# Kernel optimization log

Measured on AMD Instinct MI355X. Metric: run time of the kernel, lower is better.

Reference implementation:

```python
import jax, jax.numpy as jnp
import numpy as np


def _pairwise_l2(set1, set2):
    # set1: [B, N, C], set2: [B, M, C] -> [B, N, M] Euclidean distances.
    # Equivalent to ||a - b||_2 computed via the expanded quadratic form,
    # avoiding the O(B*N*M*C) broadcasted-difference intermediate.
    sq1 = jnp.sum(set1 * set1, axis=-1)  # [B, N]
    sq2 = jnp.sum(set2 * set2, axis=-1)  # [B, M]
    inner = jnp.einsum('bnc,bmc->bnm', set1, set2)  # [B, N, M]
    d2 = sq1[:, :, None] + sq2[:, None, :] - 2.0 * inner
    return jnp.sqrt(jnp.maximum(d2, 0.0))


def reference(set1, set2):
    # mode == Hausdorff.average
    if set1.ndim == 2:
        set1 = set1[None]
    if set2.ndim == 2:
        set2 = set2[None]
    distances = _pairwise_l2(set1, set2)  # [B, N, M]
    term_1 = jnp.mean(jnp.min(distances, axis=2), axis=1)  # [B]
    term_2 = jnp.mean(jnp.min(distances, axis=1), axis=1)  # [B]
    res = term_1 + term_2
    if res.shape[0] == 1:
        res = jnp.squeeze(res, axis=0)
    return res


def setup_inputs() -> dict:
    key = jax.random.key(0)
    k1, k2 = jax.random.split(key)
    B, N, M, C = 8, 4096, 4096, 128
    set1 = jax.random.normal(k1, (B, N, C), dtype=jnp.float32)
    set2 = jax.random.normal(k2, (B, M, C), dtype=jnp.float32)
    return {"set1": set1, "set2": set2}
```

## Files before the change

kernel.cpp:

```cpp
#include <hip/hip_runtime.h>

#define B_ 8
#define N_ 4096
#define M_ 4096
#define C_ 128
#define BN_ (B_ * N_)
#define BM_ (B_ * M_)

typedef __attribute__((ext_vector_type(8))) short bf16x8;
typedef __attribute__((ext_vector_type(4))) float floatx4;
typedef __attribute__((ext_vector_type(8))) unsigned short ushort8;

__device__ __forceinline__ unsigned short f2bf(float x) {
    unsigned int u = __float_as_uint(x);
    u += 0x7FFFu + ((u >> 16) & 1u);
    return (unsigned short)(u >> 16);
}

__device__ __forceinline__ void gl2lds16(const void* g, void* l) {
    __builtin_amdgcn_global_load_lds(
        (const __attribute__((address_space(1))) void*)g,
        (__attribute__((address_space(3))) void*)l, 16, 0, 0);
}

__global__ __launch_bounds__(256) void prep_kernel(
    const float* __restrict__ S1, const float* __restrict__ S2,
    float* __restrict__ norms, unsigned short* __restrict__ bfA,
    unsigned short* __restrict__ bfB, float* __restrict__ out) {
    const int lane = threadIdx.x & 63;
    const int w    = threadIdx.x >> 6;
    const int gw   = blockIdx.x * 4 + w;
    const int r4   = lane >> 4;
    const int g4   = lane & 15;
    const int row  = gw * 4 + r4;

    const float* src = (row < BN_) ? S1 + (size_t)row * C_
                                   : S2 + (size_t)(row - BN_) * C_;
    float4 v0 = ((const float4*)src)[g4 * 2];
    float4 v1 = ((const float4*)src)[g4 * 2 + 1];

    float s = v0.x*v0.x + v0.y*v0.y + v0.z*v0.z + v0.w*v0.w
            + v1.x*v1.x + v1.y*v1.y + v1.z*v1.z + v1.w*v1.w;
    s += __shfl_xor(s, 1, 64);
    s += __shfl_xor(s, 2, 64);
    s += __shfl_xor(s, 4, 64);
    s += __shfl_xor(s, 8, 64);

    ushort8 o;
    o[0] = f2bf(v0.x); o[1] = f2bf(v0.y); o[2] = f2bf(v0.z); o[3] = f2bf(v0.w);
    o[4] = f2bf(v1.x); o[5] = f2bf(v1.y); o[6] = f2bf(v1.z); o[7] = f2bf(v1.w);

    unsigned short* dst = (row < BN_) ? bfA + (size_t)row * C_
                                      : bfB + (size_t)(row - BN_) * C_;
    *(ushort8*)&dst[(g4 ^ (row & 15)) * 8] = o;

    if (g4 == 0) norms[row] = -0.5f * s;
    if (blockIdx.x == 0 && threadIdx.x < B_) out[threadIdx.x] = 0.f;
}

__global__ __launch_bounds__(256, 2) void hausdorff_mfma(
    const unsigned short* __restrict__ Abf, const unsigned short* __restrict__ Bbf,
    const float* __restrict__ ahalf_g, const float* __restrict__ bhalf_g,
    float* __restrict__ rowpart, float* __restrict__ colpart) {

    __shared__ unsigned short B_lds[2][64 * 128];
    __shared__ float colmax_lds[4][1024];

    const int b     = blockIdx.z;
    const int x     = blockIdx.x;
    const int panel = blockIdx.y;
    const int row0  = x * 256;
    const int tid   = threadIdx.x;
    const int lane  = tid & 63;
    const int w     = tid >> 6;
    const int lm    = lane & 15;
    const int quad  = lane >> 4;
    const int wrow  = w * 64;

    const unsigned short* Aws = Abf + ((size_t)b * N_ + row0 + wrow) * C_;
    const unsigned short* Bws = Bbf + ((size_t)b * M_ + (size_t)panel * 1024) * C_;
    const float* bhalf = bhalf_g + (size_t)b * M_ + panel * 1024;

    bf16x8 af[4][4];
    #pragma unroll
    for (int i = 0; i < 4; ++i)
        #pragma unroll
        for (int c = 0; c < 4; ++c)
            af[i][c] = *(const bf16x8*)
                &Aws[(16 * i + lm) * 128 + (((c * 4 + quad) ^ lm) * 8)];

    float ha[16];
    #pragma unroll
    for (int i = 0; i < 4; ++i) {
        float4 t = *(const float4*)&ahalf_g[(size_t)b * N_ + row0 + wrow + 16 * i + 4 * quad];
        ha[4*i+0] = t.x; ha[4*i+1] = t.y; ha[4*i+2] = t.z; ha[4*i+3] = t.w;
    }

    float rv[16];
    #pragma unroll
    for (int v = 0; v < 16; ++v) rv[v] = -1e30f;

    #pragma unroll
    for (int k = 0; k < 4; ++k) {
        const int off = w * 2048 + k * 512;
        gl2lds16(Bws + off + lane * 8, &B_lds[0][off]);
    }

    for (int it = 0; it < 16; ++it) {
        const int cur = it & 1;
        __syncthreads();

        if (it < 15) {
            const unsigned short* Bt = Bws + (size_t)(it + 1) * 64 * C_;
            #pragma unroll
            for (int k = 0; k < 4; ++k) {
                const int off = w * 2048 + k * 512;
                gl2lds16(Bt + off + lane * 8, &B_lds[cur ^ 1][off]);
            }
        }

        float hb[4];
        #pragma unroll
        for (int j = 0; j < 4; ++j)
            hb[j] = bhalf[it * 64 + 16 * j + lm];

        floatx4 acc[4][4];
        #pragma unroll
        for (int i = 0; i < 4; ++i)
            #pragma unroll
            for (int j = 0; j < 4; ++j)
                #pragma unroll
                for (int r = 0; r < 4; ++r)
                    acc[i][j][r] = ha[4 * i + r] + hb[j];

        #pragma unroll
        for (int h = 0; h < 2; ++h) {
            bf16x8 bfr[2][4];
            #pragma unroll
            for (int j2 = 0; j2 < 2; ++j2)
                #pragma unroll
                for (int c = 0; c < 4; ++c)
                    bfr[j2][c] = *(const bf16x8*)
                        &B_lds[cur][(16 * (2 * h + j2) + lm) * 128 +
                                    (((c * 4 + quad) ^ lm) * 8)];
            #pragma unroll
            for (int c = 0; c < 4; ++c)
                #pragma unroll
                for (int i = 0; i < 4; ++i)
                    #pragma unroll
                    for (int j2 = 0; j2 < 2; ++j2)
                        acc[i][2 * h + j2] = __builtin_amdgcn_mfma_f32_16x16x32_bf16(
                            af[i][c], bfr[j2][c], acc[i][2 * h + j2], 0, 0, 0);
        }

        #pragma unroll
        for (int i = 0; i < 4; ++i)
            #pragma unroll
            for (int r = 0; r < 4; ++r) {
                float m01 = fmaxf(acc[i][0][r], acc[i][1][r]);
                float m23 = fmaxf(acc[i][2][r], acc[i][3][r]);
                rv[4 * i + r] = fmaxf(rv[4 * i + r], fmaxf(m01, m23));
            }

        #pragma unroll
        for (int j = 0; j < 4; ++j) {
            float t0 = fmaxf(fmaxf(acc[0][j][0], acc[0][j][1]),
                             fmaxf(acc[0][j][2], acc[0][j][3]));
            float t1 = fmaxf(fmaxf(acc[1][j][0], acc[1][j][1]),
                             fmaxf(acc[1][j][2], acc[1][j][3]));
            float t2 = fmaxf(fmaxf(acc[2][j][0], acc[2][j][1]),
                             fmaxf(acc[2][j][2], acc[2][j][3]));
            float t3 = fmaxf(fmaxf(acc[3][j][0], acc[3][j][1]),
                             fmaxf(acc[3][j][2], acc[3][j][3]));
            float cv = fmaxf(fmaxf(t0, t1), fmaxf(t2, t3));
            cv = fmaxf(cv, __shfl_xor(cv, 16, 64));
            cv = fmaxf(cv, __shfl_xor(cv, 32, 64));
            if (quad == 0)
                colmax_lds[w][it * 64 + 16 * j + lm] = cv;
        }
    }

    #pragma unroll
    for (int s = 1; s < 16; s <<= 1)
        #pragma unroll
        for (int v = 0; v < 16; ++v)
            rv[v] = fmaxf(rv[v], __shfl_xor(rv[v], s, 64));
    if (lm == 0) {
        #pragma unroll
        for (int v = 0; v < 16; ++v)
            rowpart[((size_t)panel * B_ + b) * N_ + row0 + wrow +
                    16 * (v >> 2) + 4 * quad + (v & 3)] = rv[v];
    }

    __syncthreads();

    {
        const int c = tid * 4;
        float4 a0 = *(const float4*)&colmax_lds[0][c];
        float4 a1 = *(const float4*)&colmax_lds[1][c];
        float4 a2 = *(const float4*)&colmax_lds[2][c];
        float4 a3 = *(const float4*)&colmax_lds[3][c];
        float4 r;
        r.x = fmaxf(fmaxf(a0.x, a1.x), fmaxf(a2.x, a3.x));
        r.y = fmaxf(fmaxf(a0.y, a1.y), fmaxf(a2.y, a3.y));
        r.z = fmaxf(fmaxf(a0.z, a1.z), fmaxf(a2.z, a3.z));
        r.w = fmaxf(fmaxf(a0.w, a1.w), fmaxf(a2.w, a3.w));
        *(float4*)&colpart[((size_t)x * B_ + b) * M_ + (size_t)panel * 1024 + c] = r;
    }
}

__global__ __launch_bounds__(256) void hausdorff_reduce(
    const float* __restrict__ rowpart, const float* __restrict__ colpart,
    float* __restrict__ out) {
    __shared__ float ws4[4];
    const int b    = blockIdx.x >> 3;
    const int part = blockIdx.x & 7;
    const int base = part * 512;
    float s = 0.f;
    for (int i = base + (int)threadIdx.x; i < base + 512; i += 256) {
        float ra = fmaxf(rowpart[((size_t)0 * B_ + b) * N_ + i],
                         rowpart[((size_t)1 * B_ + b) * N_ + i]);
        float rb = fmaxf(rowpart[((size_t)2 * B_ + b) * N_ + i],
                         rowpart[((size_t)3 * B_ + b) * N_ + i]);
        float rm = fmaxf(ra, rb);
        float ca = -1e30f, cb = -1e30f;
        #pragma unroll
        for (int xx = 0; xx < 16; xx += 2) {
            ca = fmaxf(ca, colpart[((size_t)xx * B_ + b) * M_ + i]);
            cb = fmaxf(cb, colpart[((size_t)(xx + 1) * B_ + b) * M_ + i]);
        }
        float cm = fmaxf(ca, cb);
        s += sqrtf(fmaxf(-2.f * rm, 0.f)) * (1.f / N_)
           + sqrtf(fmaxf(-2.f * cm, 0.f)) * (1.f / M_);
    }
    #pragma unroll
    for (int off = 32; off > 0; off >>= 1) s += __shfl_down(s, off, 64);
    if ((threadIdx.x & 63) == 0) ws4[threadIdx.x >> 6] = s;
    __syncthreads();
    if (threadIdx.x == 0)
        atomicAdd(&out[b], ws4[0] + ws4[1] + ws4[2] + ws4[3]);
}

extern "C" void kernel_launch(void* const* d_in, const int* in_sizes, int n_in,
                              void* d_out, int out_size, void* d_ws, size_t ws_size,
                              hipStream_t stream) {
    const float* s1 = (const float*)d_in[0];
    const float* s2 = (const float*)d_in[1];
    float* out = (float*)d_out;

    float* norms         = (float*)d_ws;
    unsigned short* bfA  = (unsigned short*)(norms + BN_ + BM_);
    unsigned short* bfB  = bfA + (size_t)BN_ * C_;
    float* rowpart       = (float*)(bfB + (size_t)BM_ * C_);
    float* colpart       = rowpart + (size_t)4 * B_ * N_;

    prep_kernel<<<(BN_ + BM_) / 16, 256, 0, stream>>>(
        s1, s2, norms, bfA, bfB, out);

    dim3 grid(N_ / 256, M_ / 1024, B_);
    hausdorff_mfma<<<grid, 256, 0, stream>>>(
        bfA, bfB, norms, norms + BN_, rowpart, colpart);

    hausdorff_reduce<<<B_ * 8, 256, 0, stream>>>(rowpart, colpart, out);
}
```

Measured before the change: 121.4 us.

## Process two B tiles per barrier with 4-slot LDS ring and MFMA priority

The main loop now handles two 64-row B tiles per iteration, using a four-buffer LDS ring so each barrier covers two tiles and prefetches the next pair. MFMA sections are wrapped in s_setprio to favour matrix issue, and the prep kernel processes four rows per wave with a quarter of the blocks. The aim is fewer barriers and more latency hiding. The cost is doubled LDS for B (64KB plus colmax), which may limit occupancy to fewer than 2 blocks per CU, and more register pressure.

```diff
diff --git a/kernel.cpp b/kernel.cpp
--- a/kernel.cpp
+++ b/kernel.cpp
@@ -29,41 +29,109 @@
     unsigned short* __restrict__ bfB, float* __restrict__ out) {
     const int lane = threadIdx.x & 63;
     const int w    = threadIdx.x >> 6;
-    const int gw   = blockIdx.x * 4 + w;
     const int r4   = lane >> 4;
     const int g4   = lane & 15;
-    const int row  = gw * 4 + r4;
-
-    const float* src = (row < BN_) ? S1 + (size_t)row * C_
-                                   : S2 + (size_t)(row - BN_) * C_;
-    float4 v0 = ((const float4*)src)[g4 * 2];
-    float4 v1 = ((const float4*)src)[g4 * 2 + 1];
-
-    float s = v0.x*v0.x + v0.y*v0.y + v0.z*v0.z + v0.w*v0.w
-            + v1.x*v1.x + v1.y*v1.y + v1.z*v1.z + v1.w*v1.w;
-    s += __shfl_xor(s, 1, 64);
-    s += __shfl_xor(s, 2, 64);
-    s += __shfl_xor(s, 4, 64);
-    s += __shfl_xor(s, 8, 64);
-
-    ushort8 o;
-    o[0] = f2bf(v0.x); o[1] = f2bf(v0.y); o[2] = f2bf(v0.z); o[3] = f2bf(v0.w);
-    o[4] = f2bf(v1.x); o[5] = f2bf(v1.y); o[6] = f2bf(v1.z); o[7] = f2bf(v1.w);
-
-    unsigned short* dst = (row < BN_) ? bfA + (size_t)row * C_
-                                      : bfB + (size_t)(row - BN_) * C_;
-    *(ushort8*)&dst[(g4 ^ (row & 15)) * 8] = o;
-
-    if (g4 == 0) norms[row] = -0.5f * s;
+
+    #pragma unroll
+    for (int step = 0; step < 4; ++step) {
+        const int row = blockIdx.x * 64 + step * 16 + w * 4 + r4;
+
+        const float* src = (row < BN_) ? S1 + (size_t)row * C_
+                                       : S2 + (size_t)(row - BN_) * C_;
+        float4 v0 = ((const float4*)src)[g4 * 2];
+        float4 v1 = ((const float4*)src)[g4 * 2 + 1];
+
+        float s = v0.x*v0.x + v0.y*v0.y + v0.z*v0.z + v0.w*v0.w
+                + v1.x*v1.x + v1.y*v1.y + v1.z*v1.z + v1.w*v1.w;
+        s += __shfl_xor(s, 1, 64);
+        s += __shfl_xor(s, 2, 64);
+        s += __shfl_xor(s, 4, 64);
+        s += __shfl_xor(s, 8, 64);
+
+        ushort8 o;
+        o[0] = f2bf(v0.x); o[1] = f2bf(v0.y);
+        o[2] = f2bf(v0.z); o[3] = f2bf(v0.w);
+        o[4] = f2bf(v1.x); o[5] = f2bf(v1.y);
+        o[6] = f2bf(v1.z); o[7] = f2bf(v1.w);
+
+        unsigned short* dst = (row < BN_) ? bfA + (size_t)row * C_
+                                          : bfB + (size_t)(row - BN_) * C_;
+        *(ushort8*)&dst[(g4 ^ (row & 15)) * 8] = o;
+
+        if (g4 == 0) norms[row] = -0.5f * s;
+    }
     if (blockIdx.x == 0 && threadIdx.x < B_) out[threadIdx.x] = 0.f;
 }
+
+
+#define COMPUTE_TILE(t_, buf_)                                                \
+  do {                                                                        \
+    const int tt_ = (t_);                                                     \
+    float hb_[4];                                                             \
+    _Pragma("unroll")                                                         \
+    for (int j_ = 0; j_ < 4; ++j_)                                            \
+        hb_[j_] = bhalf[tt_ * 64 + 16 * j_ + lm];                             \
+    floatx4 acc_[4][4];                                                       \
+    _Pragma("unroll")                                                         \
+    for (int i_ = 0; i_ < 4; ++i_)                                            \
+      _Pragma("unroll")                                                       \
+      for (int j_ = 0; j_ < 4; ++j_)                                          \
+        _Pragma("unroll")                                                     \
+        for (int r_ = 0; r_ < 4; ++r_)                                        \
+            acc_[i_][j_][r_] = ha[4 * i_ + r_] + hb_[j_];                     \
+    _Pragma("unroll")                                                         \
+    for (int h_ = 0; h_ < 2; ++h_) {                                          \
+      bf16x8 bfr_[2][4];                                                      \
+      _Pragma("unroll")                                                       \
+      for (int j2_ = 0; j2_ < 2; ++j2_)                                       \
+        _Pragma("unroll")                                                     \
+        for (int c_ = 0; c_ < 4; ++c_)                                        \
+          bfr_[j2_][c_] = *(const bf16x8*)                                    \
+              &B_lds[buf_][(16 * (2 * h_ + j2_) + lm) * 128 +                 \
+                           (((c_ * 4 + quad) ^ lm) * 8)];                     \
+      __builtin_amdgcn_s_setprio(1);                                          \
+      _Pragma("unroll")                                                       \
+      for (int c_ = 0; c_ < 4; ++c_)                                          \
+        _Pragma("unroll")                                                     \
+        for (int i_ = 0; i_ < 4; ++i_)                                        \
+          _Pragma("unroll")                                                   \
+          for (int j2_ = 0; j2_ < 2; ++j2_)                                   \
+            acc_[i_][2 * h_ + j2_] = __builtin_amdgcn_mfma_f32_16x16x32_bf16( \
+                af[i_][c_], bfr_[j2_][c_], acc_[i_][2 * h_ + j2_], 0, 0, 0);  \
+      __builtin_amdgcn_s_setprio(0);                                          \
+    }                                                                         \
+    _Pragma("unroll")                                                         \
+    for (int i_ = 0; i_ < 4; ++i_)                                            \
+      _Pragma("unroll")                                                       \
+      for (int r_ = 0; r_ < 4; ++r_) {                                        \
+        float m01_ = fmaxf(acc_[i_][0][r_], acc_[i_][1][r_]);                 \
+        float m23_ = fmaxf(acc_[i_][2][r_], acc_[i_][3][r_]);                 \
+        rv[4 * i_ + r_] = fmaxf(rv[4 * i_ + r_], fmaxf(m01_, m23_));          \
+      }                                                                       \
+    _Pragma("unroll")                                                         \
+    for (int j_ = 0; j_ < 4; ++j_) {                                          \
+      float t0_ = fmaxf(fmaxf(acc_[0][j_][0], acc_[0][j_][1]),                \
+                        fmaxf(acc_[0][j_][2], acc_[0][j_][3]));               \
+      float t1_ = fmaxf(fmaxf(acc_[1][j_][0], acc_[1][j_][1]),                \
+                        fmaxf(acc_[1][j_][2], acc_[1][j_][3]));               \
+      float t2_ = fmaxf(fmaxf(acc_[2][j_][0], acc_[2][j_][1]),                \
+                        fmaxf(acc_[2][j_][2], acc_[2][j_][3]));               \
+      float t3_ = fmaxf(fmaxf(acc_[3][j_][0], acc_[3][j_][1]),                \
+                        fmaxf(acc_[3][j_][2], acc_[3][j_][3]));               \
+      float cv_ = fmaxf(fmaxf(t0_, t1_), fmaxf(t2_, t3_));                    \
+      cv_ = fmaxf(cv_, __shfl_xor(cv_, 16, 64));                              \
+      cv_ = fmaxf(cv_, __shfl_xor(cv_, 32, 64));                              \
+      if (quad == 0)                                                          \
+          colmax_lds[w][tt_ * 64 + 16 * j_ + lm] = cv_;                       \
+    }                                                                         \
+  } while (0)
 
 __global__ __launch_bounds__(256, 2) void hausdorff_mfma(
     const unsigned short* __restrict__ Abf, const unsigned short* __restrict__ Bbf,
     const float* __restrict__ ahalf_g, const float* __restrict__ bhalf_g,
     float* __restrict__ rowpart, float* __restrict__ colpart) {
 
-    __shared__ unsigned short B_lds[2][64 * 128];
+    __shared__ unsigned short B_lds[4][64 * 128];
     __shared__ float colmax_lds[4][1024];
 
     const int b     = blockIdx.z;
@@ -103,81 +171,25 @@
     #pragma unroll
     for (int k = 0; k < 4; ++k) {
         const int off = w * 2048 + k * 512;
-        gl2lds16(Bws + off + lane * 8, &B_lds[0][off]);
-    }
-
-    for (int it = 0; it < 16; ++it) {
-        const int cur = it & 1;
+        gl2lds16(Bws + off + lane * 8,        &B_lds[0][off]);
+        gl2lds16(Bws + 8192 + off + lane * 8, &B_lds[1][off]);
+    }
+
+    for (int s = 0; s < 8; ++s) {
         __syncthreads();
 
-        if (it < 15) {
-            const unsigned short* Bt = Bws + (size_t)(it + 1) * 64 * C_;
+        if (s < 7) {
+            const unsigned short* Bt = Bws + (size_t)(2 * s + 2) * 64 * C_;
             #pragma unroll
             for (int k = 0; k < 4; ++k) {
                 const int off = w * 2048 + k * 512;
-                gl2lds16(Bt + off + lane * 8, &B_lds[cur ^ 1][off]);
+                gl2lds16(Bt + off + lane * 8,        &B_lds[(2 * s + 2) & 3][off]);
+                gl2lds16(Bt + 8192 + off + lane * 8, &B_lds[(2 * s + 3) & 3][off]);
             }
         }
 
-        float hb[4];
-        #pragma unroll
-        for (int j = 0; j < 4; ++j)
-            hb[j] = bhalf[it * 64 + 16 * j + lm];
-
-        floatx4 acc[4][4];
-        #pragma unroll
-        for (int i = 0; i < 4; ++i)
-            #pragma unroll
-            for (int j = 0; j < 4; ++j)
-                #pragma unroll
-                for (int r = 0; r < 4; ++r)
-                    acc[i][j][r] = ha[4 * i + r] + hb[j];
-
-        #pragma unroll
-        for (int h = 0; h < 2; ++h) {
-            bf16x8 bfr[2][4];
-            #pragma unroll
-            for (int j2 = 0; j2 < 2; ++j2)
-                #pragma unroll
-                for (int c = 0; c < 4; ++c)
-                    bfr[j2][c] = *(const bf16x8*)
-                        &B_lds[cur][(16 * (2 * h + j2) + lm) * 128 +
-                                    (((c * 4 + quad) ^ lm) * 8)];
-            #pragma unroll
-            for (int c = 0; c < 4; ++c)
-                #pragma unroll
-                for (int i = 0; i < 4; ++i)
-                    #pragma unroll
-                    for (int j2 = 0; j2 < 2; ++j2)
-                        acc[i][2 * h + j2] = __builtin_amdgcn_mfma_f32_16x16x32_bf16(
-                            af[i][c], bfr[j2][c], acc[i][2 * h + j2], 0, 0, 0);
-        }
-
-        #pragma unroll
-        for (int i = 0; i < 4; ++i)
-            #pragma unroll
-            for (int r = 0; r < 4; ++r) {
-                float m01 = fmaxf(acc[i][0][r], acc[i][1][r]);
-                float m23 = fmaxf(acc[i][2][r], acc[i][3][r]);
-                rv[4 * i + r] = fmaxf(rv[4 * i + r], fmaxf(m01, m23));
-            }
-
-        #pragma unroll
-        for (int j = 0; j < 4; ++j) {
-            float t0 = fmaxf(fmaxf(acc[0][j][0], acc[0][j][1]),
-                             fmaxf(acc[0][j][2], acc[0][j][3]));
-            float t1 = fmaxf(fmaxf(acc[1][j][0], acc[1][j][1]),
-                             fmaxf(acc[1][j][2], acc[1][j][3]));
-            float t2 = fmaxf(fmaxf(acc[2][j][0], acc[2][j][1]),
-                             fmaxf(acc[2][j][2], acc[2][j][3]));
-            float t3 = fmaxf(fmaxf(acc[3][j][0], acc[3][j][1]),
-                             fmaxf(acc[3][j][2], acc[3][j][3]));
-            float cv = fmaxf(fmaxf(t0, t1), fmaxf(t2, t3));
-            cv = fmaxf(cv, __shfl_xor(cv, 16, 64));
-            cv = fmaxf(cv, __shfl_xor(cv, 32, 64));
-            if (quad == 0)
-                colmax_lds[w][it * 64 + 16 * j + lm] = cv;
-        }
+        COMPUTE_TILE(2 * s,     (2 * s) & 3);
+        COMPUTE_TILE(2 * s + 1, (2 * s + 1) & 3);
     }
 
     #pragma unroll
@@ -254,7 +266,7 @@
     float* rowpart       = (float*)(bfB + (size_t)BM_ * C_);
     float* colpart       = rowpart + (size_t)4 * B_ * N_;
 
-    prep_kernel<<<(BN_ + BM_) / 16, 256, 0, stream>>>(
+    prep_kernel<<<(BN_ + BM_) / 64, 256, 0, stream>>>(
         s1, s2, norms, bfA, bfB, out);
 
     dim3 grid(N_ / 256, M_ / 1024, B_);
```

New measurement: 139.8 us. 1.15x slower.

## Use LDS atomicMax for column maxima, stage bhalf in LDS, batch prep rows

Applied to the files above, without the earlier changes.

Replaces the cross-quad shuffle reduction of column maxima with LDS atomicMax on order-preserving integer keys, one slot per quad, and reduces the four slots at the end. The per-panel bhalf values are loaded once into LDS by async global-to-LDS copy instead of read from global memory every iteration. The prep kernel now processes four row groups per block with a quarter of the blocks. This trades shuffles for LDS atomics and adds an LDS zeroing step. It also relies on the bhalf LDS load being visible after the first barrier.

```diff
diff --git a/kernel.cpp b/kernel.cpp
--- a/kernel.cpp
+++ b/kernel.cpp
@@ -17,6 +17,15 @@
     return (unsigned short)(u >> 16);
 }
 
+__device__ __forceinline__ unsigned fkey(float f) {
+    unsigned u = __float_as_uint(f);
+    return u ^ (unsigned)(((int)u >> 31) | 0x80000000);
+}
+__device__ __forceinline__ float funkey(unsigned k) {
+    unsigned u = (k & 0x80000000u) ? (k ^ 0x80000000u) : ~k;
+    return __uint_as_float(u);
+}
+
 __device__ __forceinline__ void gl2lds16(const void* g, void* l) {
     __builtin_amdgcn_global_load_lds(
         (const __attribute__((address_space(1))) void*)g,
@@ -29,32 +38,37 @@
     unsigned short* __restrict__ bfB, float* __restrict__ out) {
     const int lane = threadIdx.x & 63;
     const int w    = threadIdx.x >> 6;
-    const int gw   = blockIdx.x * 4 + w;
     const int r4   = lane >> 4;
     const int g4   = lane & 15;
-    const int row  = gw * 4 + r4;
-
-    const float* src = (row < BN_) ? S1 + (size_t)row * C_
-                                   : S2 + (size_t)(row - BN_) * C_;
-    float4 v0 = ((const float4*)src)[g4 * 2];
-    float4 v1 = ((const float4*)src)[g4 * 2 + 1];
-
-    float s = v0.x*v0.x + v0.y*v0.y + v0.z*v0.z + v0.w*v0.w
-            + v1.x*v1.x + v1.y*v1.y + v1.z*v1.z + v1.w*v1.w;
-    s += __shfl_xor(s, 1, 64);
-    s += __shfl_xor(s, 2, 64);
-    s += __shfl_xor(s, 4, 64);
-    s += __shfl_xor(s, 8, 64);
-
-    ushort8 o;
-    o[0] = f2bf(v0.x); o[1] = f2bf(v0.y); o[2] = f2bf(v0.z); o[3] = f2bf(v0.w);
-    o[4] = f2bf(v1.x); o[5] = f2bf(v1.y); o[6] = f2bf(v1.z); o[7] = f2bf(v1.w);
-
-    unsigned short* dst = (row < BN_) ? bfA + (size_t)row * C_
-                                      : bfB + (size_t)(row - BN_) * C_;
-    *(ushort8*)&dst[(g4 ^ (row & 15)) * 8] = o;
-
-    if (g4 == 0) norms[row] = -0.5f * s;
+
+    #pragma unroll
+    for (int step = 0; step < 4; ++step) {
+        const int row = blockIdx.x * 64 + step * 16 + w * 4 + r4;
+
+        const float* src = (row < BN_) ? S1 + (size_t)row * C_
+                                       : S2 + (size_t)(row - BN_) * C_;
+        float4 v0 = ((const float4*)src)[g4 * 2];
+        float4 v1 = ((const float4*)src)[g4 * 2 + 1];
+
+        float s = v0.x*v0.x + v0.y*v0.y + v0.z*v0.z + v0.w*v0.w
+                + v1.x*v1.x + v1.y*v1.y + v1.z*v1.z + v1.w*v1.w;
+        s += __shfl_xor(s, 1, 64);
+        s += __shfl_xor(s, 2, 64);
+        s += __shfl_xor(s, 4, 64);
+        s += __shfl_xor(s, 8, 64);
+
+        ushort8 o;
+        o[0] = f2bf(v0.x); o[1] = f2bf(v0.y);
+        o[2] = f2bf(v0.z); o[3] = f2bf(v0.w);
+        o[4] = f2bf(v1.x); o[5] = f2bf(v1.y);
+        o[6] = f2bf(v1.z); o[7] = f2bf(v1.w);
+
+        unsigned short* dst = (row < BN_) ? bfA + (size_t)row * C_
+                                          : bfB + (size_t)(row - BN_) * C_;
+        *(ushort8*)&dst[(g4 ^ (row & 15)) * 8] = o;
+
+        if (g4 == 0) norms[row] = -0.5f * s;
+    }
     if (blockIdx.x == 0 && threadIdx.x < B_) out[threadIdx.x] = 0.f;
 }
 
@@ -64,7 +78,8 @@
     float* __restrict__ rowpart, float* __restrict__ colpart) {
 
     __shared__ unsigned short B_lds[2][64 * 128];
-    __shared__ float colmax_lds[4][1024];
+    __shared__ unsigned int colmax_u[1024][4];
+    __shared__ float bhalf_lds[1024];
 
     const int b     = blockIdx.z;
     const int x     = blockIdx.x;
@@ -79,7 +94,17 @@
 
     const unsigned short* Aws = Abf + ((size_t)b * N_ + row0 + wrow) * C_;
     const unsigned short* Bws = Bbf + ((size_t)b * M_ + (size_t)panel * 1024) * C_;
-    const float* bhalf = bhalf_g + (size_t)b * M_ + panel * 1024;
+
+    {
+        uint4 z; z.x = z.y = z.z = z.w = 0u;
+        unsigned int* cm = &colmax_u[0][0];
+        #pragma unroll
+        for (int k = 0; k < 4; ++k)
+            *(uint4*)&cm[tid * 16 + k * 4] = z;
+    }
+
+    gl2lds16(bhalf_g + (size_t)b * M_ + panel * 1024 + w * 256 + lane * 4,
+             &bhalf_lds[w * 256]);
 
     bf16x8 af[4][4];
     #pragma unroll
@@ -122,7 +147,7 @@
         float hb[4];
         #pragma unroll
         for (int j = 0; j < 4; ++j)
-            hb[j] = bhalf[it * 64 + 16 * j + lm];
+            hb[j] = bhalf_lds[it * 64 + 16 * j + lm];
 
         floatx4 acc[4][4];
         #pragma unroll
@@ -173,10 +198,7 @@
             float t3 = fmaxf(fmaxf(acc[3][j][0], acc[3][j][1]),
                              fmaxf(acc[3][j][2], acc[3][j][3]));
             float cv = fmaxf(fmaxf(t0, t1), fmaxf(t2, t3));
-            cv = fmaxf(cv, __shfl_xor(cv, 16, 64));
-            cv = fmaxf(cv, __shfl_xor(cv, 32, 64));
-            if (quad == 0)
-                colmax_lds[w][it * 64 + 16 * j + lm] = cv;
+            atomicMax(&colmax_u[it * 64 + 16 * j + lm][quad], fkey(cv));
         }
     }
 
@@ -195,17 +217,16 @@
     __syncthreads();
 
     {
-        const int c = tid * 4;
-        float4 a0 = *(const float4*)&colmax_lds[0][c];
-        float4 a1 = *(const float4*)&colmax_lds[1][c];
-        float4 a2 = *(const float4*)&colmax_lds[2][c];
-        float4 a3 = *(const float4*)&colmax_lds[3][c];
-        float4 r;
-        r.x = fmaxf(fmaxf(a0.x, a1.x), fmaxf(a2.x, a3.x));
-        r.y = fmaxf(fmaxf(a0.y, a1.y), fmaxf(a2.y, a3.y));
-        r.z = fmaxf(fmaxf(a0.z, a1.z), fmaxf(a2.z, a3.z));
-        r.w = fmaxf(fmaxf(a0.w, a1.w), fmaxf(a2.w, a3.w));
-        *(float4*)&colpart[((size_t)x * B_ + b) * M_ + (size_t)panel * 1024 + c] = r;
+        const int c0 = tid * 4;
+        float cout[4];
+        #pragma unroll
+        for (int cc = 0; cc < 4; ++cc) {
+            uint4 q = *(const uint4*)&colmax_u[c0 + cc][0];
+            unsigned k = max(max(q.x, q.y), max(q.z, q.w));
+            cout[cc] = funkey(k);
+        }
+        *(float4*)&colpart[((size_t)x * B_ + b) * M_ + (size_t)panel * 1024 + c0] =
+            *(float4*)cout;
     }
 }
 
@@ -254,7 +275,7 @@
     float* rowpart       = (float*)(bfB + (size_t)BM_ * C_);
     float* colpart       = rowpart + (size_t)4 * B_ * N_;
 
-    prep_kernel<<<(BN_ + BM_) / 16, 256, 0, stream>>>(
+    prep_kernel<<<(BN_ + BM_) / 64, 256, 0, stream>>>(
         s1, s2, norms, bfA, bfB, out);
 
     dim3 grid(N_ / 256, M_ / 1024, B_);
```

Measured after the change: 111.8 us. 1.09x faster.
